# Kernel tuning notes

Measured on AMD Instinct MI355X. Metric: run time of the kernel, lower is better.

## Reference

```python
import jax, jax.numpy as jnp
import numpy as np

B, L, J, D_MODEL, N_HIDDEN = 8, 2048, 2048, 1024, 1024


def setup_inputs() -> dict:
    key = jax.random.key(0)
    ks = jax.random.split(key, 6)
    scale = 1.0 / np.sqrt(D_MODEL)
    return {
        "q": jax.random.normal(ks[0], (B, L, D_MODEL), dtype=jnp.float32),
        "k": jax.random.normal(ks[1], (B, J, D_MODEL), dtype=jnp.float32),
        "v": jax.random.normal(ks[2], (B, J, D_MODEL), dtype=jnp.float32),
        "mask": jnp.zeros((B, L, J), dtype=jnp.float32),
        # Linear(d_model, n_hidden, bias=False) weights, stored [n_hidden, d_model] like torch
        "W_q": jax.random.normal(ks[3], (N_HIDDEN, D_MODEL), dtype=jnp.float32) * scale,
        "W_k": jax.random.normal(ks[4], (N_HIDDEN, D_MODEL), dtype=jnp.float32) * scale,
        "W_v": jax.random.normal(ks[5], (N_HIDDEN, D_MODEL), dtype=jnp.float32) * scale,
    }


def reference(q, k, v, mask, W_q, W_k, W_v):
    # Linear projections (torch Linear: x @ W.T)
    qp = jnp.einsum('bld,hd->blh', q, W_q)
    kp = jnp.einsum('bjd,hd->bjh', k, W_k)
    vp = jnp.einsum('bjd,hd->bjh', v, W_v)
    # scaled dot-product scores [B, L, J]
    scores = jnp.einsum('blh,bjh->blj', qp, kp) / jnp.sqrt(jnp.float32(N_HIDDEN)).astype(qp.dtype)
    scores = scores + mask
    attn = jax.nn.softmax(scores, axis=-1)
    return jnp.einsum('blj,bjh->blh', attn, vp)
```

## Files before the change

kernel.cpp:

```cpp
#include <hip/hip_runtime.h>
#include <hip/hip_fp16.h>

typedef _Float16 f16;
typedef __attribute__((ext_vector_type(8))) _Float16 f16x8;
typedef __attribute__((ext_vector_type(4))) _Float16 f16x4;
typedef __attribute__((ext_vector_type(4))) float f32x4;

#define BM 256
#define BN 256
#define BK 64

__device__ __forceinline__ void gll16(const void* src, void* dst) {
  __builtin_amdgcn_global_load_lds((const __attribute__((address_space(1))) void*)src,
                                   (__attribute__((address_space(3))) void*)dst,
                                   16, 0, 0);
}

template<int MODE>
__global__ __launch_bounds__(512, 2)
void gemm_bt(const f16* __restrict__ Aall, const f16* __restrict__ Ball,
             void* __restrict__ Call,
             int M, int N, int K, int lda, int ldb, int ldc,
             long strideA, long strideB, long strideC,
             const float* __restrict__ maskAll, long strideMask,
             float* __restrict__ lvec, float scale)
{
  __shared__ __align__(16) f16 smA[2][BM * BK];
  __shared__ __align__(16) f16 smB[2][BN * BK];

  unsigned gx = gridDim.x, gy = gridDim.y;
  unsigned id = (blockIdx.z * gy + blockIdx.y) * gx + blockIdx.x;
  unsigned nwg = gx * gy * gridDim.z;
  unsigned swz = (id & 7) * (nwg >> 3) + (id >> 3);
  unsigned bx = swz % gx, rem = swz / gx;
  unsigned by = rem % gy, bz = rem / gy;

  const int z = bz;
  const f16* A = Aall + (long)z * strideA;
  const f16* B = Ball + (long)z * strideB;

  const int tid  = threadIdx.x;
  const int wid  = tid >> 6;
  const int lane = tid & 63;
  const int wm = wid >> 2;
  const int wn = wid & 3;
  const int lr = lane & 15;
  const int g  = lane >> 4;

  const long brow = (long)by * BM;
  const long bcol = (long)bx * BN;
  const int  nt   = K / BK;

  f32x4 acc[8][4] = {};
  f16x8 af[8], bf[8];

  auto stage_half = [&](f16* dst, const f16* src, long prow, int ld_, int rowOff, int t) {
    #pragma unroll
    for (int i = 0; i < 2; ++i) {
      int c  = i * 512 + tid;
      int r  = c >> 3;
      int sl = (c & 7) ^ (r & 7);
      gll16(src + (prow + rowOff + r) * (long)ld_ + t * BK + sl * 8,
            dst + rowOff * BK + c * 8);
    }
  };
  auto rdA = [&](const f16* sa, int mh) {
    #pragma unroll
    for (int fm = 0; fm < 4; ++fm)
      #pragma unroll
      for (int ks = 0; ks < 2; ++ks) {
        int r = wm * 128 + mh * 64 + fm * 16 + lr;
        af[fm * 2 + ks] = *(const f16x8*)(sa + r * BK + ((ks * 4 + g) ^ (r & 7)) * 8);
      }
  };
  auto rdB = [&](const f16* sb, int nh) {
    #pragma unroll
    for (int fn = 0; fn < 2; ++fn)
      #pragma unroll
      for (int ks = 0; ks < 2; ++ks) {
        int r = wn * 64 + (nh * 2 + fn) * 16 + lr;
        bf[(nh * 2 + fn) * 2 + ks] = *(const f16x8*)(sb + r * BK + ((ks * 4 + g) ^ (r & 7)) * 8);
      }
  };
  auto sync_mfma = [&](int fm0, int fn0) {
    __builtin_amdgcn_s_barrier();
    asm volatile("s_waitcnt lgkmcnt(0)" ::: "memory");
    __builtin_amdgcn_sched_barrier(0);
    __builtin_amdgcn_s_setprio(1);
    #pragma unroll
    for (int fm = 0; fm < 4; ++fm)
      #pragma unroll
      for (int fn = 0; fn < 2; ++fn)
        #pragma unroll
        for (int ks = 0; ks < 2; ++ks)
          acc[fm0 + fm][fn0 + fn] = __builtin_amdgcn_mfma_f32_16x16x32_f16(
              af[fm * 2 + ks], bf[(fn0 + fn) * 2 + ks], acc[fm0 + fm][fn0 + fn], 0, 0, 0);
    __builtin_amdgcn_s_setprio(0);
    __builtin_amdgcn_s_barrier();
  };

  stage_half(smA[0], A, brow, lda, 0, 0);
  stage_half(smA[0], A, brow, lda, 128, 0);
  stage_half(smB[0], B, bcol, ldb, 0, 0);
  stage_half(smB[0], B, bcol, ldb, 128, 0);
  stage_half(smB[1], B, bcol, ldb, 0, 1);
  stage_half(smB[1], B, bcol, ldb, 128, 1);
  asm volatile("s_waitcnt vmcnt(4)" ::: "memory");
  __builtin_amdgcn_s_barrier();

  const int niter = nt / 2;
  for (int i = 0; i < niter; ++i) {
    const bool last = (i == niter - 1);
    const int t2 = 2 * i + 2, t3 = 2 * i + 3;

    rdA(smA[0], 0); rdB(smB[0], 0);
    stage_half(smA[1], A, brow, lda, 0, 2 * i + 1);
    sync_mfma(0, 0);
    rdB(smB[0], 1);
    stage_half(smA[1], A, brow, lda, 128, 2 * i + 1);
    sync_mfma(0, 2);
    rdA(smA[0], 1);
    if (t2 < nt) stage_half(smB[0], B, bcol, ldb, 0, t2);
    sync_mfma(4, 2);
    if (t2 < nt) stage_half(smB[0], B, bcol, ldb, 128, t2);
    if (!last) { asm volatile("s_waitcnt vmcnt(4)" ::: "memory"); }
    else       { asm volatile("s_waitcnt vmcnt(0)" ::: "memory"); }
    sync_mfma(4, 0);
    rdA(smA[1], 0); rdB(smB[1], 0);
    if (t2 < nt) stage_half(smA[0], A, brow, lda, 0, t2);
    sync_mfma(0, 0);
    rdB(smB[1], 1);
    if (t2 < nt) stage_half(smA[0], A, brow, lda, 128, t2);
    sync_mfma(0, 2);
    rdA(smA[1], 1);
    if (t3 < nt) stage_half(smB[1], B, bcol, ldb, 0, t3);
    sync_mfma(4, 2);
    if (t3 < nt) stage_half(smB[1], B, bcol, ldb, 128, t3);
    if (!last) { asm volatile("s_waitcnt vmcnt(4)" ::: "memory"); }
    sync_mfma(4, 0);
  }

  const int rb = (lane >> 4) * 4;

  if (MODE == 0) {
    f16* C = (f16*)Call + (long)z * strideC;
    #pragma unroll
    for (int m = 0; m < 8; ++m)
      #pragma unroll
      for (int j = 0; j < 4; ++j) {
        long grow = brow + wm * 128 + m * 16 + rb + j;
        #pragma unroll
        for (int n = 0; n < 4; ++n) {
          long gcol = bcol + wn * 64 + n * 16 + lr;
          C[grow * ldc + gcol] = (f16)acc[m][n][j];
        }
      }
  } else if (MODE == 1) {
    f16* C = (f16*)Call + (long)z * strideC;
    const float* mask = maskAll + (long)z * strideMask;
    #pragma unroll
    for (int m = 0; m < 8; ++m)
      #pragma unroll
      for (int j = 0; j < 4; ++j) {
        long grow = brow + wm * 128 + m * 16 + rb + j;
        float s = 0.f;
        #pragma unroll
        for (int n = 0; n < 4; ++n) {
          long gcol = bcol + wn * 64 + n * 16 + lr;
          float p = __expf(acc[m][n][j] * scale + mask[grow * ldc + gcol]);
          C[grow * ldc + gcol] = (f16)p;
          s += p;
        }
        s += __shfl_xor(s, 1);
        s += __shfl_xor(s, 2);
        s += __shfl_xor(s, 4);
        s += __shfl_xor(s, 8);
        if (lr == 0)
          lvec[((long)z * M + grow) * 32 + bx * 4 + wn] = s;
      }
  } else {
    float* C = (float*)Call + (long)z * strideC;
    #pragma unroll
    for (int m = 0; m < 8; ++m)
      #pragma unroll
      for (int j = 0; j < 4; ++j) {
        long grow = brow + wm * 128 + m * 16 + rb + j;
        float inv = 1.0f / lvec[(long)z * M + grow];
        #pragma unroll
        for (int n = 0; n < 4; ++n) {
          long gcol = bcol + wn * 64 + n * 16 + lr;
          C[grow * ldc + gcol] = acc[m][n][j] * inv;
        }
      }
  }
}

__global__ void cvt_all(const float* __restrict__ q, const float* __restrict__ k,
                        const float* __restrict__ v, const float* __restrict__ Wq,
                        const float* __restrict__ Wk, const float* __restrict__ Wv,
                        f16* __restrict__ qf, f16* __restrict__ kf, f16* __restrict__ vf,
                        f16* __restrict__ Wqf, f16* __restrict__ Wkf, f16* __restrict__ Wvf)
{
  const long NQ4 = 4194304, NW4 = 262144;
  const long total = 3 * NQ4 + 3 * NW4;
  for (long i = (long)blockIdx.x * blockDim.x + threadIdx.x; i < total;
       i += (long)gridDim.x * blockDim.x) {
    const float* src; f16* dst; long j = i;
    if      (j <     NQ4)           { src = q;  dst = qf; }
    else if (j < 2 * NQ4)           { src = k;  dst = kf;  j -= NQ4; }
    else if (j < 3 * NQ4)           { src = v;  dst = vf;  j -= 2 * NQ4; }
    else if (j < 3 * NQ4 + NW4)     { src = Wq; dst = Wqf; j -= 3 * NQ4; }
    else if (j < 3 * NQ4 + 2 * NW4) { src = Wk; dst = Wkf; j -= 3 * NQ4 + NW4; }
    else                            { src = Wv; dst = Wvf; j -= 3 * NQ4 + 2 * NW4; }
    float4 vv = ((const float4*)src)[j];
    f16x4 o;
    o[0] = (f16)vv.x; o[1] = (f16)vv.y; o[2] = (f16)vv.z; o[3] = (f16)vv.w;
    ((f16x4*)dst)[j] = o;
  }
}

__global__ void reduce_l(const float* __restrict__ lpart, float* __restrict__ lsum, int n) {
  int i = blockIdx.x * blockDim.x + threadIdx.x;
  if (i < n) {
    float s = 0.f;
    #pragma unroll
    for (int j = 0; j < 32; ++j) s += lpart[(long)i * 32 + j];
    lsum[i] = s;
  }
}

extern "C" void kernel_launch(void* const* d_in, const int* in_sizes, int n_in,
                              void* d_out, int out_size, void* d_ws, size_t ws_size,
                              hipStream_t stream)
{
  const float* q    = (const float*)d_in[0];
  const float* k    = (const float*)d_in[1];
  const float* v    = (const float*)d_in[2];
  const float* mask = (const float*)d_in[3];
  const float* Wq   = (const float*)d_in[4];
  const float* Wk   = (const float*)d_in[5];
  const float* Wv   = (const float*)d_in[6];
  float* out = (float*)d_out;
  char*  ws  = (char*)d_ws;

  f16* qf  = (f16*)(ws + 0);
  f16* kf  = (f16*)(ws + 33554432);
  f16* vf  = (f16*)(ws + 67108864);
  f16* Pm  = (f16*)(ws + 0);
  f16* Wqf = (f16*)(ws + 100663296);
  f16* Wkf = (f16*)(ws + 102760448);
  f16* Wvf = (f16*)(ws + 104857600);
  f16* qp  = (f16*)(ws + 106954752);
  f16* kp  = (f16*)(ws + 140509184);
  f16* vpT = (f16*)(ws + 174063616);
  float* lpart = (float*)(ws + 207618048);
  float* lsum  = (float*)(ws + 209715200);

  const long L = 2048, J = 2048, D = 1024, H = 1024;

  cvt_all<<<dim3(2048), dim3(256), 0, stream>>>(q, k, v, Wq, Wk, Wv, qf, kf, vf, Wqf, Wkf, Wvf);

  gemm_bt<0><<<dim3(1024 / BN, 16384 / BM, 1), dim3(512), 0, stream>>>(
      qf, Wqf, qp, 16384, 1024, 1024, 1024, 1024, 1024,
      0, 0, 0, nullptr, 0, nullptr, 0.f);
  gemm_bt<0><<<dim3(1024 / BN, 16384 / BM, 1), dim3(512), 0, stream>>>(
      kf, Wkf, kp, 16384, 1024, 1024, 1024, 1024, 1024,
      0, 0, 0, nullptr, 0, nullptr, 0.f);
  gemm_bt<0><<<dim3(2048 / BN, 1024 / BM, 8), dim3(512), 0, stream>>>(
      Wvf, vf, vpT, 1024, 2048, 1024, 1024, 1024, 2048,
      0, J * D, H * J, nullptr, 0, nullptr, 0.f);

  gemm_bt<1><<<dim3(2048 / BN, 2048 / BM, 8), dim3(512), 0, stream>>>(
      qp, kp, Pm, 2048, 2048, 1024, 1024, 1024, 2048,
      L * H, J * H, L * J, mask, L * J, lpart, 0.03125f);

  reduce_l<<<dim3(16384 / 256), dim3(256), 0, stream>>>(lpart, lsum, 16384);

  gemm_bt<2><<<dim3(1024 / BN, 2048 / BM, 8), dim3(512), 0, stream>>>(
      Pm, vpT, out, 2048, 1024, 2048, 2048, 2048, 1024,
      L * J, H * J, L * H, nullptr, 0, lsum, 0.f);
}
```

Baseline: 377.0 us.

## Fuse fp32-to-fp16 input conversion into projection GEMM tile loads

Drops the separate conversion kernel. The three projection GEMMs now read fp32 q/k/v and weights directly, convert them to fp16 in registers, and store them to LDS with ordinary stores instead of async global-to-LDS loads. This removes a full write and re-read of the converted inputs through HBM. In exchange the loads become synchronous register round-trips, and the vmcnt waits are removed from the pipelined loop, which weakens the overlap of loads with MFMA work and doubles global bytes read per tile.

```diff
diff --git a/kernel.cpp b/kernel.cpp
--- a/kernel.cpp
+++ b/kernel.cpp
@@ -16,9 +16,9 @@
                                    16, 0, 0);
 }
 
-template<int MODE>
+template<int MODE, bool CVT>
 __global__ __launch_bounds__(512, 2)
-void gemm_bt(const f16* __restrict__ Aall, const f16* __restrict__ Ball,
+void gemm_bt(const void* __restrict__ Aall, const void* __restrict__ Ball,
              void* __restrict__ Call,
              int M, int N, int K, int lda, int ldb, int ldc,
              long strideA, long strideB, long strideC,
@@ -36,8 +36,8 @@
   unsigned by = rem % gy, bz = rem / gy;
 
   const int z = bz;
-  const f16* A = Aall + (long)z * strideA;
-  const f16* B = Ball + (long)z * strideB;
+  const void* A = (const char*)Aall + (long)z * strideA * (CVT ? 4 : 2);
+  const void* B = (const char*)Ball + (long)z * strideB * (CVT ? 4 : 2);
 
   const int tid  = threadIdx.x;
   const int wid  = tid >> 6;
@@ -54,14 +54,24 @@
   f32x4 acc[8][4] = {};
   f16x8 af[8], bf[8];
 
-  auto stage_half = [&](f16* dst, const f16* src, long prow, int ld_, int rowOff, int t) {
+  auto stage_half = [&](f16* dst, const void* srcBase, long prow, int ld_, int rowOff, int t) {
     #pragma unroll
     for (int i = 0; i < 2; ++i) {
       int c  = i * 512 + tid;
       int r  = c >> 3;
       int sl = (c & 7) ^ (r & 7);
-      gll16(src + (prow + rowOff + r) * (long)ld_ + t * BK + sl * 8,
-            dst + rowOff * BK + c * 8);
+      long off = (prow + rowOff + r) * (long)ld_ + t * BK + sl * 8;
+      if constexpr (CVT) {
+        const float* s = (const float*)srcBase + off;
+        float4 lo = *(const float4*)s;
+        float4 hi = *(const float4*)(s + 4);
+        f16x8 o;
+        o[0] = (f16)lo.x; o[1] = (f16)lo.y; o[2] = (f16)lo.z; o[3] = (f16)lo.w;
+        o[4] = (f16)hi.x; o[5] = (f16)hi.y; o[6] = (f16)hi.z; o[7] = (f16)hi.w;
+        *(f16x8*)(dst + rowOff * BK + c * 8) = o;
+      } else {
+        gll16((const f16*)srcBase + off, dst + rowOff * BK + c * 8);
+      }
     }
   };
   auto rdA = [&](const f16* sa, int mh) {
@@ -105,7 +115,8 @@
   stage_half(smB[0], B, bcol, ldb, 128, 0);
   stage_half(smB[1], B, bcol, ldb, 0, 1);
   stage_half(smB[1], B, bcol, ldb, 128, 1);
-  asm volatile("s_waitcnt vmcnt(4)" ::: "memory");
+  if constexpr (!CVT) { asm volatile("s_waitcnt vmcnt(4)" ::: "memory"); }
+  else                { asm volatile("s_waitcnt lgkmcnt(0)" ::: "memory"); }
   __builtin_amdgcn_s_barrier();
 
   const int niter = nt / 2;
@@ -123,8 +134,10 @@
     if (t2 < nt) stage_half(smB[0], B, bcol, ldb, 0, t2);
     sync_mfma(4, 2);
     if (t2 < nt) stage_half(smB[0], B, bcol, ldb, 128, t2);
-    if (!last) { asm volatile("s_waitcnt vmcnt(4)" ::: "memory"); }
-    else       { asm volatile("s_waitcnt vmcnt(0)" ::: "memory"); }
+    if constexpr (!CVT) {
+      if (!last) { asm volatile("s_waitcnt vmcnt(4)" ::: "memory"); }
+      else       { asm volatile("s_waitcnt vmcnt(0)" ::: "memory"); }
+    }
     sync_mfma(4, 0);
     rdA(smA[1], 0); rdB(smB[1], 0);
     if (t2 < nt) stage_half(smA[0], A, brow, lda, 0, t2);
@@ -136,7 +149,9 @@
     if (t3 < nt) stage_half(smB[1], B, bcol, ldb, 0, t3);
     sync_mfma(4, 2);
     if (t3 < nt) stage_half(smB[1], B, bcol, ldb, 128, t3);
-    if (!last) { asm volatile("s_waitcnt vmcnt(4)" ::: "memory"); }
+    if constexpr (!CVT) {
+      if (!last) { asm volatile("s_waitcnt vmcnt(4)" ::: "memory"); }
+    }
     sync_mfma(4, 0);
   }
 
@@ -192,30 +207,6 @@
           C[grow * ldc + gcol] = acc[m][n][j] * inv;
         }
       }
-  }
-}
-
-__global__ void cvt_all(const float* __restrict__ q, const float* __restrict__ k,
-                        const float* __restrict__ v, const float* __restrict__ Wq,
-                        const float* __restrict__ Wk, const float* __restrict__ Wv,
-                        f16* __restrict__ qf, f16* __restrict__ kf, f16* __restrict__ vf,
-                        f16* __restrict__ Wqf, f16* __restrict__ Wkf, f16* __restrict__ Wvf)
-{
-  const long NQ4 = 4194304, NW4 = 262144;
-  const long total = 3 * NQ4 + 3 * NW4;
-  for (long i = (long)blockIdx.x * blockDim.x + threadIdx.x; i < total;
-       i += (long)gridDim.x * blockDim.x) {
-    const float* src; f16* dst; long j = i;
-    if      (j <     NQ4)           { src = q;  dst = qf; }
-    else if (j < 2 * NQ4)           { src = k;  dst = kf;  j -= NQ4; }
-    else if (j < 3 * NQ4)           { src = v;  dst = vf;  j -= 2 * NQ4; }
-    else if (j < 3 * NQ4 + NW4)     { src = Wq; dst = Wqf; j -= 3 * NQ4; }
-    else if (j < 3 * NQ4 + 2 * NW4) { src = Wk; dst = Wkf; j -= 3 * NQ4 + NW4; }
-    else                            { src = Wv; dst = Wvf; j -= 3 * NQ4 + 2 * NW4; }
-    float4 vv = ((const float4*)src)[j];
-    f16x4 o;
-    o[0] = (f16)vv.x; o[1] = (f16)vv.y; o[2] = (f16)vv.z; o[3] = (f16)vv.w;
-    ((f16x4*)dst)[j] = o;
   }
 }
 
@@ -243,40 +234,32 @@
   float* out = (float*)d_out;
   char*  ws  = (char*)d_ws;
 
-  f16* qf  = (f16*)(ws + 0);
-  f16* kf  = (f16*)(ws + 33554432);
-  f16* vf  = (f16*)(ws + 67108864);
-  f16* Pm  = (f16*)(ws + 0);
-  f16* Wqf = (f16*)(ws + 100663296);
-  f16* Wkf = (f16*)(ws + 102760448);
-  f16* Wvf = (f16*)(ws + 104857600);
-  f16* qp  = (f16*)(ws + 106954752);
-  f16* kp  = (f16*)(ws + 140509184);
-  f16* vpT = (f16*)(ws + 174063616);
-  float* lpart = (float*)(ws + 207618048);
-  float* lsum  = (float*)(ws + 209715200);
+  f16*   Pm    = (f16*)(ws + 0);
+  f16*   qp    = (f16*)(ws + 67108864);
+  f16*   kp    = (f16*)(ws + 100663296);
+  f16*   vpT   = (f16*)(ws + 134217728);
+  float* lpart = (float*)(ws + 167772160);
+  float* lsum  = (float*)(ws + 169869312);
 
   const long L = 2048, J = 2048, D = 1024, H = 1024;
 
-  cvt_all<<<dim3(2048), dim3(256), 0, stream>>>(q, k, v, Wq, Wk, Wv, qf, kf, vf, Wqf, Wkf, Wvf);
-
-  gemm_bt<0><<<dim3(1024 / BN, 16384 / BM, 1), dim3(512), 0, stream>>>(
-      qf, Wqf, qp, 16384, 1024, 1024, 1024, 1024, 1024,
+  gemm_bt<0, true><<<dim3(1024 / BN, 16384 / BM, 1), dim3(512), 0, stream>>>(
+      q, Wq, qp, 16384, 1024, 1024, 1024, 1024, 1024,
       0, 0, 0, nullptr, 0, nullptr, 0.f);
-  gemm_bt<0><<<dim3(1024 / BN, 16384 / BM, 1), dim3(512), 0, stream>>>(
-      kf, Wkf, kp, 16384, 1024, 1024, 1024, 1024, 1024,
+  gemm_bt<0, true><<<dim3(1024 / BN, 16384 / BM, 1), dim3(512), 0, stream>>>(
+      k, Wk, kp, 16384, 1024, 1024, 1024, 1024, 1024,
       0, 0, 0, nullptr, 0, nullptr, 0.f);
-  gemm_bt<0><<<dim3(2048 / BN, 1024 / BM, 8), dim3(512), 0, stream>>>(
-      Wvf, vf, vpT, 1024, 2048, 1024, 1024, 1024, 2048,
+  gemm_bt<0, true><<<dim3(2048 / BN, 1024 / BM, 8), dim3(512), 0, stream>>>(
+      Wv, v, vpT, 1024, 2048, 1024, 1024, 1024, 2048,
       0, J * D, H * J, nullptr, 0, nullptr, 0.f);
 
-  gemm_bt<1><<<dim3(2048 / BN, 2048 / BM, 8), dim3(512), 0, stream>>>(
+  gemm_bt<1, false><<<dim3(2048 / BN, 2048 / BM, 8), dim3(512), 0, stream>>>(
       qp, kp, Pm, 2048, 2048, 1024, 1024, 1024, 2048,
       L * H, J * H, L * J, mask, L * J, lpart, 0.03125f);
 
   reduce_l<<<dim3(16384 / 256), dim3(256), 0, stream>>>(lpart, lsum, 16384);
 
-  gemm_bt<2><<<dim3(1024 / BN, 2048 / BM, 8), dim3(512), 0, stream>>>(
+  gemm_bt<2, false><<<dim3(1024 / BN, 2048 / BM, 8), dim3(512), 0, stream>>>(
       Pm, vpT, out, 2048, 1024, 2048, 2048, 2048, 1024,
       L * J, H * J, L * H, nullptr, 0, lsum, 0.f);
 }
```

New measurement: 453.8 us. 1.2x slower.
